# Optimization experiments

Hardware: AMD Instinct MI355X
Metric: run time of the kernel (lower is better)

Reference implementation:

```python
import jax, jax.numpy as jnp
import numpy as np

N_NODES = 100000


def spmm(edge_src, edge_dst, edge_val, x):
    """z[dst] += val * x[src] over all edges (COO sparse-dense matmul)."""
    gathered = edge_val[:, None] * x[edge_src]  # [E, d]
    return jax.ops.segment_sum(gathered, edge_dst, num_segments=N_NODES)


def setup_inputs() -> dict:
    key = jax.random.key(0)
    k1, k2, k3, k4, k5, k6 = jax.random.split(key, 6)
    N, E, IN, H, C = N_NODES, 1600000, 256, 128, 40
    features = jax.random.normal(k1, (N, IN), dtype=jnp.float32)
    # xavier_uniform-like init
    b1 = float(np.sqrt(6.0 / (IN + H)))
    b2 = float(np.sqrt(6.0 / (H + C)))
    W1 = jax.random.uniform(k2, (IN, H), dtype=jnp.float32, minval=-b1, maxval=b1)
    W2 = jax.random.uniform(k3, (H, C), dtype=jnp.float32, minval=-b2, maxval=b2)
    edge_src = jax.random.randint(k4, (E,), 0, N, dtype=jnp.int32)
    edge_dst = jnp.sort(jax.random.randint(k5, (E,), 0, N, dtype=jnp.int32))
    # normalized-adjacency-like positive edge weights
    edge_val = jax.random.uniform(k6, (E,), dtype=jnp.float32)
    return {"features": features, "W1": W1, "W2": W2,
            "edge_src": edge_src, "edge_dst": edge_dst, "edge_val": edge_val}


def reference(features, W1, W2, edge_src, edge_dst, edge_val):
    # Decoupled GCN: all dense NN layers first (relu between, none after last) ...
    h = jax.nn.relu(features @ W1)
    h = h @ W2  # [N, num_classes]
    # ... then nlayers (=2) rounds of graph propagation (spmm aggregation)
    h = spmm(edge_src, edge_dst, edge_val, h)
    h = spmm(edge_src, edge_dst, edge_val, h)
    return h
```

## Files before the change

kernel.cpp:

```cpp
#include <hip/hip_runtime.h>
#include <cstddef>
#include <cstdint>

#define IN_DIM 256
#define H_DIM  128
#define C_DIM  40
#define BM     128
#define LDA    264
#define LDH    136
#define PAD_C  40
#define W2_ROWS 64
#define STEP   512

typedef short bf16x8 __attribute__((ext_vector_type(8)));
typedef float f32x16 __attribute__((ext_vector_type(16)));
typedef uint  u32x4  __attribute__((ext_vector_type(4)));

__device__ __forceinline__ ushort f2bf(float f) {
  uint u = __builtin_bit_cast(uint, f);
  u += 0x7fffu + ((u >> 16) & 1u);
  return (ushort)(u >> 16);
}
__device__ __forceinline__ float bf2f(uint s) {
  uint u = s << 16;
  return __builtin_bit_cast(float, u);
}
__device__ __forceinline__ uint pack2bf(float a, float b) {
#if __has_builtin(__builtin_amdgcn_cvt_pk_bf16_f32)
  typedef __bf16 bf16v2 __attribute__((ext_vector_type(2)));
  bf16v2 r = __builtin_amdgcn_cvt_pk_bf16_f32(a, b);
  return __builtin_bit_cast(uint, r);
#else
  return (uint)f2bf(a) | ((uint)f2bf(b) << 16);
#endif
}

__global__ void setup_kernel(const int* __restrict__ dst, int E,
                             int* __restrict__ row_ptr, int N,
                             const float* __restrict__ W1,
                             const float* __restrict__ W2,
                             ushort* __restrict__ b_frag,
                             ushort* __restrict__ w2t) {
  int tid = blockIdx.x * blockDim.x + threadIdx.x;
  if (tid < E) {
    int d1 = dst[tid];
    int d0 = (tid == 0) ? -1 : dst[tid - 1];
    for (int v = d0 + 1; v <= d1; ++v) row_ptr[v] = tid;
    if (tid == E - 1)
      for (int v = d1 + 1; v <= N; ++v) row_ptr[v] = E;
    return;
  }
  int u = tid - E;
  if (u < 4096) {
    int l = u & 63, ks = (u >> 6) & 15, tn = u >> 10;
    int n  = 32 * tn + (l & 31);
    int k0 = ks * 16 + ((l >> 5) << 3);
    ushort r[8];
#pragma unroll
    for (int j = 0; j < 8; ++j) r[j] = f2bf(W1[(k0 + j) * H_DIM + n]);
    *(uint4*)(b_frag + u * 8) = *(uint4*)r;
    return;
  }
  u -= 4096;
  if (u < W2_ROWS * H_DIM) {
    int n = u >> 7, k = u & 127;
    w2t[u] = (n < C_DIM) ? f2bf(W2[k * C_DIM + n]) : (ushort)0;
  }
}

__global__ __launch_bounds__(256, 2) void fused_dense_kernel(
    const float* __restrict__ feat, const ushort* __restrict__ b_frag,
    const ushort* __restrict__ w2t, ushort* __restrict__ z0, int N) {
  __shared__ __align__(16) ushort smem[128 * LDA];

  const int t = threadIdx.x;
  const int w = t >> 6, l = t & 63;
  const int nb = blockIdx.x * BM;

  f32x16 acc[4];
#pragma unroll
  for (int tn = 0; tn < 4; ++tn)
#pragma unroll
    for (int r = 0; r < 16; ++r) acc[tn][r] = 0.f;

  const ushort* bp = b_frag + l * 8;
  bf16x8 Bx[2][4];
#pragma unroll
  for (int tn = 0; tn < 4; ++tn)
    Bx[0][tn] = *(const bf16x8*)(bp + tn * (16 * STEP));

#pragma unroll
  for (int c = 0; c < 32; ++c) {
    int row = 4 * c + w;
    int grow = nb + row; if (grow >= N) grow = N - 1;
    float4 v = *(const float4*)(feat + (size_t)grow * IN_DIM + l * 4);
    uint2 pk;
    pk.x = pack2bf(v.x, v.y);
    pk.y = pack2bf(v.z, v.w);
    *(uint2*)(smem + row * LDA + l * 4) = pk;
  }
  __syncthreads();

  const ushort* Abase = smem + (w * 32 + (l & 31)) * LDA + ((l >> 5) << 3);
#pragma unroll
  for (int ks = 0; ks < 16; ++ks) {
    const int c = ks & 1;
    if (ks < 15) {
#pragma unroll
      for (int tn = 0; tn < 4; ++tn)
        Bx[c ^ 1][tn] = *(const bf16x8*)(bp + tn * (16 * STEP) + (ks + 1) * STEP);
    }
    bf16x8 af = *(const bf16x8*)(Abase + ks * 16);
#pragma unroll
    for (int tn = 0; tn < 4; ++tn)
      acc[tn] = __builtin_amdgcn_mfma_f32_32x32x16_bf16(af, Bx[c][tn], acc[tn], 0, 0, 0);
  }
  __syncthreads();

#pragma unroll
  for (int tn = 0; tn < 4; ++tn) {
    int col = tn * 32 + (l & 31);
#pragma unroll
    for (int r = 0; r < 16; ++r) {
      int nodeLoc = (r & 3) + 8 * (r >> 2) + 4 * (l >> 5) + 32 * w;
      float v = acc[tn][r];
      smem[nodeLoc * LDH + col] = f2bf(v > 0.f ? v : 0.f);
    }
  }
  {
    int row = t >> 2, c4 = (t & 3) << 5;
    const uint4* src = (const uint4*)(w2t + row * H_DIM + c4);
    uint4* dst = (uint4*)(smem + 128 * LDH + row * LDH + c4);
    dst[0] = src[0];
    dst[1] = src[1];
    dst[2] = src[2];
    dst[3] = src[3];
  }
  __syncthreads();

  f32x16 acc2[2];
#pragma unroll
  for (int tn = 0; tn < 2; ++tn)
#pragma unroll
    for (int r = 0; r < 16; ++r) acc2[tn][r] = 0.f;

  const ushort* Hbase  = smem + (w * 32 + (l & 31)) * LDH + ((l >> 5) << 3);
  const ushort* W2base = smem + 128 * LDH + (l & 31) * LDH + ((l >> 5) << 3);
#pragma unroll
  for (int kb = 0; kb < 8; ++kb) {
    bf16x8 af = *(const bf16x8*)(Hbase + kb * 16);
#pragma unroll
    for (int tn = 0; tn < 2; ++tn) {
      bf16x8 bfr = *(const bf16x8*)(W2base + tn * 32 * LDH + kb * 16);
      acc2[tn] = __builtin_amdgcn_mfma_f32_32x32x16_bf16(af, bfr, acc2[tn], 0, 0, 0);
    }
  }

#pragma unroll
  for (int tn = 0; tn < 2; ++tn) {
    int col = tn * 32 + (l & 31);
    if (col < C_DIM) {
#pragma unroll
      for (int r = 0; r < 16; ++r) {
        int node = nb + 32 * w + (r & 3) + 8 * (r >> 2) + 4 * (l >> 5);
        if (node < N) z0[(size_t)node * PAD_C + col] = f2bf(acc2[tn][r]);
      }
    }
  }
}

__global__ __launch_bounds__(256) void spmm_kernel(
    const int* __restrict__ row_ptr, const int* __restrict__ esrc,
    const float* __restrict__ eval, const ushort* __restrict__ x,
    ushort* __restrict__ zb, float* __restrict__ zf, int N, int out_f32) {
  int node = (blockIdx.x << 2) + (threadIdx.x >> 6);
  if (node >= N) return;
  const int lane = threadIdx.x & 63;
  const int h = lane >> 3;
  const int j = lane & 7;
  const bool act = (j < 5);

  int e   = row_ptr[node];
  int end = row_ptr[node + 1];

  float acc[8];
#pragma unroll
  for (int c = 0; c < 8; ++c) acc[c] = 0.f;

  for (; e + 16 <= end; e += 16) {
    int   s0 = esrc[e + h];
    int   s1 = esrc[e + 8 + h];
    float v0 = eval[e + h];
    float v1 = eval[e + 8 + h];
    if (act) {
      u32x4 a = *(const u32x4*)(x + (size_t)s0 * PAD_C + j * 8);
      u32x4 b = *(const u32x4*)(x + (size_t)s1 * PAD_C + j * 8);
      acc[0] = fmaf(v0, bf2f(a.x & 0xffffu), acc[0]);
      acc[1] = fmaf(v0, bf2f(a.x >> 16),     acc[1]);
      acc[2] = fmaf(v0, bf2f(a.y & 0xffffu), acc[2]);
      acc[3] = fmaf(v0, bf2f(a.y >> 16),     acc[3]);
      acc[4] = fmaf(v0, bf2f(a.z & 0xffffu), acc[4]);
      acc[5] = fmaf(v0, bf2f(a.z >> 16),     acc[5]);
      acc[6] = fmaf(v0, bf2f(a.w & 0xffffu), acc[6]);
      acc[7] = fmaf(v0, bf2f(a.w >> 16),     acc[7]);
      acc[0] = fmaf(v1, bf2f(b.x & 0xffffu), acc[0]);
      acc[1] = fmaf(v1, bf2f(b.x >> 16),     acc[1]);
      acc[2] = fmaf(v1, bf2f(b.y & 0xffffu), acc[2]);
      acc[3] = fmaf(v1, bf2f(b.y >> 16),     acc[3]);
      acc[4] = fmaf(v1, bf2f(b.z & 0xffffu), acc[4]);
      acc[5] = fmaf(v1, bf2f(b.z >> 16),     acc[5]);
      acc[6] = fmaf(v1, bf2f(b.w & 0xffffu), acc[6]);
      acc[7] = fmaf(v1, bf2f(b.w >> 16),     acc[7]);
    }
  }
  for (; e + 8 <= end; e += 8) {
    int   s = esrc[e + h];
    float v = eval[e + h];
    if (act) {
      u32x4 u = *(const u32x4*)(x + (size_t)s * PAD_C + j * 8);
      acc[0] = fmaf(v, bf2f(u.x & 0xffffu), acc[0]);
      acc[1] = fmaf(v, bf2f(u.x >> 16),     acc[1]);
      acc[2] = fmaf(v, bf2f(u.y & 0xffffu), acc[2]);
      acc[3] = fmaf(v, bf2f(u.y >> 16),     acc[3]);
      acc[4] = fmaf(v, bf2f(u.z & 0xffffu), acc[4]);
      acc[5] = fmaf(v, bf2f(u.z >> 16),     acc[5]);
      acc[6] = fmaf(v, bf2f(u.w & 0xffffu), acc[6]);
      acc[7] = fmaf(v, bf2f(u.w >> 16),     acc[7]);
    }
  }
  if (e < end) {
    int ei = e + h;
    int ec = ei < end ? ei : end - 1;
    int   s  = esrc[ec];
    float v0 = eval[ec];
    float v  = ei < end ? v0 : 0.f;
    if (act) {
      u32x4 u = *(const u32x4*)(x + (size_t)s * PAD_C + j * 8);
      acc[0] = fmaf(v, bf2f(u.x & 0xffffu), acc[0]);
      acc[1] = fmaf(v, bf2f(u.x >> 16),     acc[1]);
      acc[2] = fmaf(v, bf2f(u.y & 0xffffu), acc[2]);
      acc[3] = fmaf(v, bf2f(u.y >> 16),     acc[3]);
      acc[4] = fmaf(v, bf2f(u.z & 0xffffu), acc[4]);
      acc[5] = fmaf(v, bf2f(u.z >> 16),     acc[5]);
      acc[6] = fmaf(v, bf2f(u.w & 0xffffu), acc[6]);
      acc[7] = fmaf(v, bf2f(u.w >> 16),     acc[7]);
    }
  }

#pragma unroll
  for (int c = 0; c < 8; ++c) acc[c] += __shfl_xor(acc[c], 8);
#pragma unroll
  for (int c = 0; c < 8; ++c) acc[c] += __shfl_xor(acc[c], 16);
#pragma unroll
  for (int c = 0; c < 8; ++c) acc[c] += __shfl_xor(acc[c], 32);

  if (out_f32) {
    if (lane < 5) {
      float4 o0 = {acc[0], acc[1], acc[2], acc[3]};
      float4 o1 = {acc[4], acc[5], acc[6], acc[7]};
      float* p = zf + (size_t)node * C_DIM + j * 8;
      *(float4*)(p + 0) = o0;
      *(float4*)(p + 4) = o1;
    }
  } else {
    if (lane < 5) {
      uint4 p;
      p.x = (uint)f2bf(acc[0]) | ((uint)f2bf(acc[1]) << 16);
      p.y = (uint)f2bf(acc[2]) | ((uint)f2bf(acc[3]) << 16);
      p.z = (uint)f2bf(acc[4]) | ((uint)f2bf(acc[5]) << 16);
      p.w = (uint)f2bf(acc[6]) | ((uint)f2bf(acc[7]) << 16);
      *(uint4*)(zb + (size_t)node * PAD_C + j * 8) = p;
    }
  }
}

extern "C" void kernel_launch(void* const* d_in, const int* in_sizes, int n_in,
                              void* d_out, int out_size, void* d_ws, size_t ws_size,
                              hipStream_t stream) {
  const float* feat  = (const float*)d_in[0];
  const float* W1    = (const float*)d_in[1];
  const float* W2    = (const float*)d_in[2];
  const int*   esrc  = (const int*)d_in[3];
  const int*   edst  = (const int*)d_in[4];
  const float* evalp = (const float*)d_in[5];
  float* out = (float*)d_out;

  const int N = in_sizes[0] / IN_DIM;
  const int E = in_sizes[3];

  const int nblk = (N + BM - 1) / BM;

  char* ws = (char*)d_ws;
  ushort* z0     = (ushort*)ws;
  ushort* z1     = (ushort*)(ws + (size_t)N * PAD_C * 2);
  ushort* b_frag = (ushort*)(ws + (size_t)N * PAD_C * 4);
  ushort* w2t    = b_frag + 4 * 16 * STEP;
  int* row_ptr   = (int*)(w2t + W2_ROWS * H_DIM);

  const int setup_items = E + 4096 + W2_ROWS * H_DIM;
  setup_kernel<<<(setup_items + 255) / 256, 256, 0, stream>>>(
      edst, E, row_ptr, N, W1, W2, b_frag, w2t);
  fused_dense_kernel<<<nblk, 256, 0, stream>>>(feat, b_frag, w2t, z0, N);
  spmm_kernel<<<(N + 3) / 4, 256, 0, stream>>>(row_ptr, esrc, evalp, z0, z1, nullptr, N, 0);
  spmm_kernel<<<(N + 3) / 4, 256, 0, stream>>>(row_ptr, esrc, evalp, z1, nullptr, out, N, 1);
}
```

Before: 275.3 us.

## Give each wave a private LDS slab and load W2 fragments from global

Each wave now loads its own 32 feature rows into a private LDS slab, so the three block-wide barriers in the fused dense kernel are removed. W2 is pre-packed into MFMA fragment order in setup and read straight from global/L2 instead of being staged through shared memory. This removes barrier stalls and the W2 LDS copy, at the cost of per-wave row-strided feature loads with less cross-wave coalescing and repeated global reads of W2 fragments. Waves writing H into their slab rely on the slab only being reused by the same wave.

```diff
diff --git a/kernel.cpp b/kernel.cpp
--- a/kernel.cpp
+++ b/kernel.cpp
@@ -9,7 +9,6 @@
 #define LDA    264
 #define LDH    136
 #define PAD_C  40
-#define W2_ROWS 64
 #define STEP   512
 
 typedef short bf16x8 __attribute__((ext_vector_type(8)));
@@ -40,7 +39,7 @@
                              const float* __restrict__ W1,
                              const float* __restrict__ W2,
                              ushort* __restrict__ b_frag,
-                             ushort* __restrict__ w2t) {
+                             ushort* __restrict__ w2f) {
   int tid = blockIdx.x * blockDim.x + threadIdx.x;
   if (tid < E) {
     int d1 = dst[tid];
@@ -62,20 +61,28 @@
     return;
   }
   u -= 4096;
-  if (u < W2_ROWS * H_DIM) {
-    int n = u >> 7, k = u & 127;
-    w2t[u] = (n < C_DIM) ? f2bf(W2[k * C_DIM + n]) : (ushort)0;
+  if (u < 1024) {
+    int l = u & 63, kt = u >> 6;
+    int tn = kt & 1, kb = kt >> 1;
+    int n  = 32 * tn + (l & 31);
+    int k0 = kb * 16 + ((l >> 5) << 3);
+    ushort r[8];
+#pragma unroll
+    for (int j = 0; j < 8; ++j)
+      r[j] = (n < C_DIM) ? f2bf(W2[(k0 + j) * C_DIM + n]) : (ushort)0;
+    *(uint4*)(w2f + u * 8) = *(uint4*)r;
   }
 }
 
 __global__ __launch_bounds__(256, 2) void fused_dense_kernel(
     const float* __restrict__ feat, const ushort* __restrict__ b_frag,
-    const ushort* __restrict__ w2t, ushort* __restrict__ z0, int N) {
+    const ushort* __restrict__ w2f, ushort* __restrict__ z0, int N) {
   __shared__ __align__(16) ushort smem[128 * LDA];
 
   const int t = threadIdx.x;
   const int w = t >> 6, l = t & 63;
   const int nb = blockIdx.x * BM;
+  ushort* slab = smem + w * (32 * LDA);
 
   f32x16 acc[4];
 #pragma unroll
@@ -91,17 +98,15 @@
 
 #pragma unroll
   for (int c = 0; c < 32; ++c) {
-    int row = 4 * c + w;
-    int grow = nb + row; if (grow >= N) grow = N - 1;
+    int grow = nb + 32 * w + c; if (grow >= N) grow = N - 1;
     float4 v = *(const float4*)(feat + (size_t)grow * IN_DIM + l * 4);
     uint2 pk;
     pk.x = pack2bf(v.x, v.y);
     pk.y = pack2bf(v.z, v.w);
-    *(uint2*)(smem + row * LDA + l * 4) = pk;
-  }
-  __syncthreads();
-
-  const ushort* Abase = smem + (w * 32 + (l & 31)) * LDA + ((l >> 5) << 3);
+    *(uint2*)(slab + c * LDA + l * 4) = pk;
+  }
+
+  const ushort* Abase = slab + (l & 31) * LDA + ((l >> 5) << 3);
 #pragma unroll
   for (int ks = 0; ks < 16; ++ks) {
     const int c = ks & 1;
@@ -115,28 +120,17 @@
     for (int tn = 0; tn < 4; ++tn)
       acc[tn] = __builtin_amdgcn_mfma_f32_32x32x16_bf16(af, Bx[c][tn], acc[tn], 0, 0, 0);
   }
-  __syncthreads();
 
 #pragma unroll
   for (int tn = 0; tn < 4; ++tn) {
     int col = tn * 32 + (l & 31);
 #pragma unroll
     for (int r = 0; r < 16; ++r) {
-      int nodeLoc = (r & 3) + 8 * (r >> 2) + 4 * (l >> 5) + 32 * w;
+      int nl = (r & 3) + 8 * (r >> 2) + 4 * (l >> 5);
       float v = acc[tn][r];
-      smem[nodeLoc * LDH + col] = f2bf(v > 0.f ? v : 0.f);
-    }
-  }
-  {
-    int row = t >> 2, c4 = (t & 3) << 5;
-    const uint4* src = (const uint4*)(w2t + row * H_DIM + c4);
-    uint4* dst = (uint4*)(smem + 128 * LDH + row * LDH + c4);
-    dst[0] = src[0];
-    dst[1] = src[1];
-    dst[2] = src[2];
-    dst[3] = src[3];
-  }
-  __syncthreads();
+      slab[nl * LDH + col] = f2bf(v > 0.f ? v : 0.f);
+    }
+  }
 
   f32x16 acc2[2];
 #pragma unroll
@@ -144,14 +138,14 @@
 #pragma unroll
     for (int r = 0; r < 16; ++r) acc2[tn][r] = 0.f;
 
-  const ushort* Hbase  = smem + (w * 32 + (l & 31)) * LDH + ((l >> 5) << 3);
-  const ushort* W2base = smem + 128 * LDH + (l & 31) * LDH + ((l >> 5) << 3);
+  const ushort* Hbase = slab + (l & 31) * LDH + ((l >> 5) << 3);
+  const ushort* wp = w2f + l * 8;
 #pragma unroll
   for (int kb = 0; kb < 8; ++kb) {
     bf16x8 af = *(const bf16x8*)(Hbase + kb * 16);
 #pragma unroll
     for (int tn = 0; tn < 2; ++tn) {
-      bf16x8 bfr = *(const bf16x8*)(W2base + tn * 32 * LDH + kb * 16);
+      bf16x8 bfr = *(const bf16x8*)(wp + (kb * 2 + tn) * STEP);
       acc2[tn] = __builtin_amdgcn_mfma_f32_32x32x16_bf16(af, bfr, acc2[tn], 0, 0, 0);
     }
   }
@@ -294,13 +288,13 @@
   ushort* z0     = (ushort*)ws;
   ushort* z1     = (ushort*)(ws + (size_t)N * PAD_C * 2);
   ushort* b_frag = (ushort*)(ws + (size_t)N * PAD_C * 4);
-  ushort* w2t    = b_frag + 4 * 16 * STEP;
-  int* row_ptr   = (int*)(w2t + W2_ROWS * H_DIM);
-
-  const int setup_items = E + 4096 + W2_ROWS * H_DIM;
+  ushort* w2f    = b_frag + 4 * 16 * STEP;
+  int* row_ptr   = (int*)(w2f + 16 * STEP);
+
+  const int setup_items = E + 4096 + 1024;
   setup_kernel<<<(setup_items + 255) / 256, 256, 0, stream>>>(
-      edst, E, row_ptr, N, W1, W2, b_frag, w2t);
-  fused_dense_kernel<<<nblk, 256, 0, stream>>>(feat, b_frag, w2t, z0, N);
+      edst, E, row_ptr, N, W1, W2, b_frag, w2f);
+  fused_dense_kernel<<<nblk, 256, 0, stream>>>(feat, b_frag, w2f, z0, N);
   spmm_kernel<<<(N + 3) / 4, 256, 0, stream>>>(row_ptr, esrc, evalp, z0, z1, nullptr, N, 0);
   spmm_kernel<<<(N + 3) / 4, 256, 0, stream>>>(row_ptr, esrc, evalp, z1, nullptr, out, N, 1);
 }
```

After: 273.7 us. About the same (-0.6%).
